# Optimization experiments

Measured on AMD Instinct MI355X. Metric: run time of the kernel, lower is better.

## Reference

```python
import jax, jax.numpy as jnp
import numpy as np

N_SRC1, N_DST1, N_DST2 = 200000, 50000, 10000
E1, E2 = 2000000, 400000
IN_F, H_F, N_CLS = 128, 256, 47


def setup_inputs() -> dict:
    key = jax.random.key(0)
    ks = jax.random.split(key, 10)
    x = jax.random.normal(ks[0], (N_SRC1, IN_F), dtype=jnp.float32)
    W_self1 = jax.random.normal(ks[1], (IN_F, H_F), dtype=jnp.float32) * (1.0 / np.sqrt(IN_F))
    W_neigh1 = jax.random.normal(ks[2], (IN_F, H_F), dtype=jnp.float32) * (1.0 / np.sqrt(IN_F))
    b1 = jnp.zeros((H_F,), dtype=jnp.float32)
    W_self2 = jax.random.normal(ks[3], (H_F, N_CLS), dtype=jnp.float32) * (1.0 / np.sqrt(H_F))
    W_neigh2 = jax.random.normal(ks[4], (H_F, N_CLS), dtype=jnp.float32) * (1.0 / np.sqrt(H_F))
    b2 = jnp.zeros((N_CLS,), dtype=jnp.float32)
    src1 = jax.random.randint(ks[5], (E1,), 0, N_SRC1, dtype=jnp.int64)
    dst1 = jnp.sort(jax.random.randint(ks[6], (E1,), 0, N_DST1, dtype=jnp.int64))
    src2 = jax.random.randint(ks[7], (E2,), 0, N_DST1, dtype=jnp.int64)
    dst2 = jnp.sort(jax.random.randint(ks[8], (E2,), 0, N_DST2, dtype=jnp.int64))
    return {"x": x, "W_self1": W_self1, "W_neigh1": W_neigh1, "b1": b1,
            "W_self2": W_self2, "W_neigh2": W_neigh2, "b2": b2,
            "src1": src1, "dst1": dst1, "src2": src2, "dst2": dst2,
            "n_dst1": N_DST1, "n_dst2": N_DST2}


def _sage_mean(h_src, h_dst, src, dst, n_dst, W_self, W_neigh, b):
    # mean neighbor aggregation: gather src feats, segment-sum onto dst, divide by in-degree
    msum = jax.ops.segment_sum(h_src[src], dst, num_segments=n_dst)  # [n_dst, F]
    deg = jax.ops.segment_sum(jnp.ones(src.shape, h_src.dtype), dst, num_segments=n_dst)
    h_neigh = msum / jnp.maximum(deg, 1.0)[:, None]
    return h_dst @ W_self + h_neigh @ W_neigh + b


def reference(x, W_self1, W_neigh1, b1, W_self2, W_neigh2, b2,
              src1, dst1, src2, dst2, n_dst1, n_dst2):
    # layer 1 (dst nodes are the prefix of src nodes, DGL MFG convention)
    h = _sage_mean(x, x[:n_dst1], src1, dst1, n_dst1, W_self1, W_neigh1, b1)
    h = jax.nn.relu(h)  # dropout = identity (eval mode)
    # layer 2
    out = _sage_mean(h, h[:n_dst2], src2, dst2, n_dst2, W_self2, W_neigh2, b2)
    return out
```

## Files before the change

kernel.cpp:

```cpp
#include <hip/hip_runtime.h>

constexpr int N_DST1 = 50000;
constexpr int N_DST2 = 10000;
constexpr int E1     = 2000000;
constexpr int E2     = 400000;
constexpr int IN_F   = 128;
constexpr int H_F    = 256;
constexpr int N_CLS  = 47;

constexpr size_t RP1_OFF = 0;
constexpr size_t RP2_OFF = 204800;
constexpr size_t BPS_OFF = 245760;
constexpr size_t BPN_OFF = 311296;
constexpr size_t BP2_OFF = 376832;
constexpr size_t X8_OFF  = 430080;
constexpr size_t HN1_OFF = 26030080;
constexpr size_t HB_OFF  = 38830080;
constexpr size_t H8_OFF  = 64430080;
constexpr size_t HN2_OFF = 77230080;

using f32x4  = __attribute__((ext_vector_type(4))) float;
using f32x2  = __attribute__((ext_vector_type(2))) float;
using short8 = __attribute__((ext_vector_type(8))) short;

__device__ __forceinline__ ushort f2bf(float f) {
    union { float f; unsigned u; } v; v.f = f;
    unsigned u = v.u;
    return (ushort)((u + 0x7fffu + ((u >> 16) & 1u)) >> 16);
}
__device__ __forceinline__ float bflo(unsigned p) {
    union { unsigned u; float f; } v; v.u = p << 16; return v.f;
}
__device__ __forceinline__ float bfhi(unsigned p) {
    union { unsigned u; float f; } v; v.u = p & 0xffff0000u; return v.f;
}

__global__ __launch_bounds__(256) void cast_x8(const float* __restrict__ x,
                                               unsigned char* __restrict__ x8) {
    int i = blockIdx.x * 256 + threadIdx.x;
    float4 v0 = ((const float4*)x)[2 * i];
    float4 v1 = ((const float4*)x)[2 * i + 1];
    int p0 = __builtin_amdgcn_cvt_pk_fp8_f32(v0.x, v0.y, 0, false);
    p0     = __builtin_amdgcn_cvt_pk_fp8_f32(v0.z, v0.w, p0, true);
    int p1 = __builtin_amdgcn_cvt_pk_fp8_f32(v1.x, v1.y, 0, false);
    p1     = __builtin_amdgcn_cvt_pk_fp8_f32(v1.z, v1.w, p1, true);
    uint2 o; o.x = (unsigned)p0; o.y = (unsigned)p1;
    ((uint2*)x8)[i] = o;
}

__global__ __launch_bounds__(256) void pack_all(
    const float* __restrict__ Ws1, const float* __restrict__ Wn1,
    const float* __restrict__ Ws2, const float* __restrict__ Wn2,
    ushort* __restrict__ bps, ushort* __restrict__ bpn,
    ushort* __restrict__ bp2) {
    int b = blockIdx.x;
    if (b < 32) {
        const float* W = (b < 16) ? Ws1 : Wn1;
        ushort* P      = (b < 16) ? bps : bpn;
        int idx = (b & 15) * 256 + threadIdx.x;
        int lane = idx & 63, kb = (idx >> 6) & 3, nb = idx >> 8;
        int n  = nb * 16 + (lane & 15);
        int k0 = kb * 32 + ((lane >> 4) * 8);
        ushort tmp[8];
#pragma unroll
        for (int j = 0; j < 8; ++j) tmp[j] = f2bf(W[(k0 + j) * H_F + n]);
        ((uint4*)P)[idx] = *(uint4*)tmp;
    } else {
        int idx = (b - 32) * 256 + threadIdx.x;
        int lane = idx & 63, rem = idx >> 6;
        int nb = rem % 3, kb = rem / 3;
        int col = nb * 16 + (lane & 15);
        int k0  = (kb & 7) * 32 + ((lane >> 4) * 8);
        const float* W = (kb < 8) ? Ws2 : Wn2;
        ushort tmp[8];
#pragma unroll
        for (int j = 0; j < 8; ++j)
            tmp[j] = (col < N_CLS) ? f2bf(W[(k0 + j) * N_CLS + col]) : (ushort)0;
        ((uint4*)bp2)[(kb * 3 + nb) * 64 + lane] = *(uint4*)tmp;
    }
}

__global__ void rowptr_all(const int* __restrict__ dst1,
                           const int* __restrict__ dst2,
                           int* __restrict__ rp1, int* __restrict__ rp2) {
    int idx = blockIdx.x * blockDim.x + threadIdx.x;
    const int* dst; int* rp; int E; int target;
    if (idx <= N_DST1) { dst = dst1; rp = rp1; E = E1; target = idx; }
    else if (idx <= N_DST1 + 1 + N_DST2) {
        dst = dst2; rp = rp2; E = E2; target = idx - (N_DST1 + 1);
    } else return;
    int lo = 0, hi = E;
    while (lo < hi) {
        int mid = (lo + hi) >> 1;
        if (dst[mid] < target) lo = mid + 1; else hi = mid;
    }
    rp[target] = lo;
}

__global__ __launch_bounds__(64) void agg1b(const unsigned char* __restrict__ x8,
                                            const int* __restrict__ src,
                                            const int* __restrict__ rp,
                                            ushort* __restrict__ hn) {
    int d = blockIdx.x, t = threadIdx.x;
    int s = rp[d], e = rp[d + 1];
    const ushort* xr = (const ushort*)x8;
    float a0 = 0.f, a1 = 0.f;
    for (int base = s; base < e; base += 64) {
        int rem = e - base;
        int n = rem < 64 ? rem : 64;
        int idx = src[base + (t < rem ? t : 0)];
        int j = 0;
        for (; j + 8 <= n; j += 8) {
            ushort u[8];
#pragma unroll
            for (int q = 0; q < 8; ++q) {
                int sq = __shfl(idx, j + q);
                u[q] = xr[sq * 64 + t];
            }
#pragma unroll
            for (int q = 0; q < 8; ++q) {
                f32x2 f = __builtin_amdgcn_cvt_pk_f32_fp8((int)u[q], false);
                a0 += f[0]; a1 += f[1];
            }
        }
        for (; j < n; ++j) {
            int sq = __shfl(idx, j);
            f32x2 f = __builtin_amdgcn_cvt_pk_f32_fp8((int)xr[sq * 64 + t], false);
            a0 += f[0]; a1 += f[1];
        }
    }
    float inv = 1.f / fmaxf((float)(e - s), 1.f);
    ((unsigned*)hn)[d * 64 + t] =
        (unsigned)f2bf(a0 * inv) | ((unsigned)f2bf(a1 * inv) << 16);
}

__global__ __launch_bounds__(64) void agg2b(const unsigned char* __restrict__ h8,
                                            const int* __restrict__ src,
                                            const int* __restrict__ rp,
                                            ushort* __restrict__ hn) {
    int d = blockIdx.x, t = threadIdx.x;
    int s = rp[d], e = rp[d + 1];
    const unsigned* hr = (const unsigned*)h8;
    float a0 = 0.f, a1 = 0.f, a2 = 0.f, a3 = 0.f;
    for (int base = s; base < e; base += 64) {
        int rem = e - base;
        int n = rem < 64 ? rem : 64;
        int idx = src[base + (t < rem ? t : 0)];
        int j = 0;
        for (; j + 4 <= n; j += 4) {
            unsigned u[4];
#pragma unroll
            for (int q = 0; q < 4; ++q) {
                int sq = __shfl(idx, j + q);
                u[q] = hr[sq * 64 + t];
            }
#pragma unroll
            for (int q = 0; q < 4; ++q) {
                f32x2 f0 = __builtin_amdgcn_cvt_pk_f32_fp8((int)u[q], false);
                f32x2 f1 = __builtin_amdgcn_cvt_pk_f32_fp8((int)u[q], true);
                a0 += f0[0]; a1 += f0[1]; a2 += f1[0]; a3 += f1[1];
            }
        }
        for (; j < n; ++j) {
            int sq = __shfl(idx, j);
            unsigned u = hr[sq * 64 + t];
            f32x2 f0 = __builtin_amdgcn_cvt_pk_f32_fp8((int)u, false);
            f32x2 f1 = __builtin_amdgcn_cvt_pk_f32_fp8((int)u, true);
            a0 += f0[0]; a1 += f0[1]; a2 += f1[0]; a3 += f1[1];
        }
    }
    float inv = 1.f / fmaxf((float)(e - s), 1.f);
    uint2 o;
    o.x = (unsigned)f2bf(a0 * inv) | ((unsigned)f2bf(a1 * inv) << 16);
    o.y = (unsigned)f2bf(a2 * inv) | ((unsigned)f2bf(a3 * inv) << 16);
    ((uint2*)hn)[d * 64 + t] = o;
}

__global__ __launch_bounds__(256) void gemm1_mfma(
    const float* __restrict__ x, const ushort* __restrict__ hn1,
    const ushort* __restrict__ BpS, const ushort* __restrict__ BpN,
    const float* __restrict__ b1, ushort* __restrict__ hb,
    unsigned char* __restrict__ h8) {
    __shared__ ushort bsm[16 * 64 * 8];
    int tid = threadIdx.x;
    int wave = tid >> 6, lane = tid & 63;
    int m0 = (blockIdx.x * 4 + wave) * 16;
    int mrow = m0 + (lane & 15);
    bool active = (m0 < N_DST1);
    if (mrow >= N_DST1) mrow = 0;
    int koff = (lane >> 4) * 8;

    f32x4 acc[16];
#pragma unroll
    for (int nb = 0; nb < 16; ++nb) acc[nb] = (f32x4){0.f, 0.f, 0.f, 0.f};

    for (int ph = 0; ph < 2; ++ph) {
        const uint4* Pg = (const uint4*)((ph == 0) ? BpS : BpN);
        const float*  Af = x   + (size_t)mrow * IN_F;
        const ushort* Ah = hn1 + (size_t)mrow * IN_F;
        for (int kb = 0; kb < 4; ++kb) {
            __syncthreads();
#pragma unroll
            for (int i = 0; i < 4; ++i) {
                int u = tid + 256 * i;
                int nb = u >> 6, l6 = u & 63;
                ((uint4*)bsm)[u] = Pg[(nb * 4 + kb) * 64 + l6];
            }
            __syncthreads();
            short8 a;
            if (ph == 0) {
                float4 a0 = *(const float4*)(Af + kb * 32 + koff);
                float4 a1 = *(const float4*)(Af + kb * 32 + koff + 4);
                a[0] = (short)f2bf(a0.x); a[1] = (short)f2bf(a0.y);
                a[2] = (short)f2bf(a0.z); a[3] = (short)f2bf(a0.w);
                a[4] = (short)f2bf(a1.x); a[5] = (short)f2bf(a1.y);
                a[6] = (short)f2bf(a1.z); a[7] = (short)f2bf(a1.w);
            } else {
                a = *(const short8*)(Ah + kb * 32 + koff);
            }
#pragma unroll
            for (int nb = 0; nb < 16; ++nb) {
                short8 b = *(const short8*)&bsm[(nb * 64 + lane) * 8];
                acc[nb] = __builtin_amdgcn_mfma_f32_16x16x32_bf16(a, b, acc[nb], 0, 0, 0);
            }
        }
    }
    if (!active) return;
    int crow0 = m0 + (lane >> 4) * 4;
    int ccol  = lane & 15;
#pragma unroll
    for (int nb = 0; nb < 16; ++nb) {
        float bias = b1[nb * 16 + ccol];
#pragma unroll
        for (int r = 0; r < 4; ++r) {
            int row = crow0 + r;
            if (row < N_DST1) {
                float v = fmaxf(acc[nb][r] + bias, 0.f);
                size_t col = (size_t)nb * 16 + ccol;
                hb[(size_t)row * H_F + col] = f2bf(v);
                int p = __builtin_amdgcn_cvt_pk_fp8_f32(v, v, 0, false);
                h8[(size_t)row * H_F + col] = (unsigned char)(p & 0xff);
            }
        }
    }
}

__global__ __launch_bounds__(256) void gemm2_mfma(
    const ushort* __restrict__ hb, const ushort* __restrict__ hn2,
    const ushort* __restrict__ P2, const float* __restrict__ b2,
    float* __restrict__ out) {
    int tid = threadIdx.x;
    int wave = tid >> 6, lane = tid & 63;
    int m0 = (blockIdx.x * 4 + wave) * 16;
    if (m0 >= N_DST2) return;
    int mrow = m0 + (lane & 15);
    int koff = (lane >> 4) * 8;

    f32x4 acc[3];
#pragma unroll
    for (int nb = 0; nb < 3; ++nb) acc[nb] = (f32x4){0.f, 0.f, 0.f, 0.f};

#pragma unroll
    for (int kb = 0; kb < 16; ++kb) {
        const ushort* A = (kb < 8)
            ? (hb  + (size_t)mrow * H_F + kb * 32 + koff)
            : (hn2 + (size_t)mrow * H_F + (kb - 8) * 32 + koff);
        short8 a = *(const short8*)A;
#pragma unroll
        for (int nb = 0; nb < 3; ++nb) {
            short8 b = *(const short8*)(P2 + ((size_t)(kb * 3 + nb) * 64 + lane) * 8);
            acc[nb] = __builtin_amdgcn_mfma_f32_16x16x32_bf16(a, b, acc[nb], 0, 0, 0);
        }
    }
    int crow0 = m0 + (lane >> 4) * 4;
    int ccol  = lane & 15;
#pragma unroll
    for (int nb = 0; nb < 3; ++nb) {
        int col = nb * 16 + ccol;
        if (col < N_CLS) {
            float bias = b2[col];
#pragma unroll
            for (int r = 0; r < 4; ++r)
                out[(size_t)(crow0 + r) * N_CLS + col] = acc[nb][r] + bias;
        }
    }
}

extern "C" void kernel_launch(void* const* d_in, const int* in_sizes, int n_in,
                              void* d_out, int out_size, void* d_ws, size_t ws_size,
                              hipStream_t stream) {
    const float* x   = (const float*)d_in[0];
    const float* Ws1 = (const float*)d_in[1];
    const float* Wn1 = (const float*)d_in[2];
    const float* b1  = (const float*)d_in[3];
    const float* Ws2 = (const float*)d_in[4];
    const float* Wn2 = (const float*)d_in[5];
    const float* b2  = (const float*)d_in[6];
    const int* src1  = (const int*)d_in[7];
    const int* dst1  = (const int*)d_in[8];
    const int* src2  = (const int*)d_in[9];
    const int* dst2  = (const int*)d_in[10];
    float* out = (float*)d_out;

    char* ws = (char*)d_ws;
    int*           rp1 = (int*)(ws + RP1_OFF);
    int*           rp2 = (int*)(ws + RP2_OFF);
    ushort*        bps = (ushort*)(ws + BPS_OFF);
    ushort*        bpn = (ushort*)(ws + BPN_OFF);
    ushort*        bp2 = (ushort*)(ws + BP2_OFF);
    unsigned char* x8  = (unsigned char*)(ws + X8_OFF);
    ushort*        hn1 = (ushort*)(ws + HN1_OFF);
    ushort*        hb  = (ushort*)(ws + HB_OFF);
    unsigned char* h8  = (unsigned char*)(ws + H8_OFF);
    ushort*        hn2 = (ushort*)(ws + HN2_OFF);

    cast_x8<<<200000 * IN_F / 8 / 256, 256, 0, stream>>>(x, x8);
    pack_all<<<44, 256, 0, stream>>>(Ws1, Wn1, Ws2, Wn2, bps, bpn, bp2);
    rowptr_all<<<(N_DST1 + N_DST2 + 2 + 255) / 256, 256, 0, stream>>>(dst1, dst2, rp1, rp2);
    agg1b<<<N_DST1, 64, 0, stream>>>(x8, src1, rp1, hn1);
    gemm1_mfma<<<(N_DST1 / 16 + 3) / 4, 256, 0, stream>>>(x, hn1, bps, bpn, b1, hb, h8);
    agg2b<<<N_DST2, 64, 0, stream>>>(h8, src2, rp2, hn2);
    gemm2_mfma<<<(N_DST2 / 16 + 3) / 4, 256, 0, stream>>>(hb, hn2, bp2, b2, out);
}
```

Measured before the change: 311.6 us.

## Merge setup kernels and gather two neighbors per wave with wider loads

The cast, weight-pack and row-pointer kernels are merged into one launch, which removes two kernel launches and their gaps. Both aggregation kernels now split the 64-lane wave into two halves. Each half gathers a different neighbor's row using wider per-lane loads (4 or 8 bytes) and reads src indices directly instead of through shuffles, and the two halves are combined with a cross-half shuffle at the end. This is meant to issue fewer, wider memory requests and keep more gathers in flight per wave. The cost is a final reduction step, and half of the wave sits idle when a node has an odd degree.

Result: no change. 306.6 us (-1.6%).

```diff
diff --git a/kernel.cpp b/kernel.cpp
--- a/kernel.cpp
+++ b/kernel.cpp
@@ -28,73 +28,71 @@
     unsigned u = v.u;
     return (ushort)((u + 0x7fffu + ((u >> 16) & 1u)) >> 16);
 }
-__device__ __forceinline__ float bflo(unsigned p) {
-    union { unsigned u; float f; } v; v.u = p << 16; return v.f;
-}
-__device__ __forceinline__ float bfhi(unsigned p) {
-    union { unsigned u; float f; } v; v.u = p & 0xffff0000u; return v.f;
-}
-
-__global__ __launch_bounds__(256) void cast_x8(const float* __restrict__ x,
-                                               unsigned char* __restrict__ x8) {
-    int i = blockIdx.x * 256 + threadIdx.x;
-    float4 v0 = ((const float4*)x)[2 * i];
-    float4 v1 = ((const float4*)x)[2 * i + 1];
-    int p0 = __builtin_amdgcn_cvt_pk_fp8_f32(v0.x, v0.y, 0, false);
-    p0     = __builtin_amdgcn_cvt_pk_fp8_f32(v0.z, v0.w, p0, true);
-    int p1 = __builtin_amdgcn_cvt_pk_fp8_f32(v1.x, v1.y, 0, false);
-    p1     = __builtin_amdgcn_cvt_pk_fp8_f32(v1.z, v1.w, p1, true);
-    uint2 o; o.x = (unsigned)p0; o.y = (unsigned)p1;
-    ((uint2*)x8)[i] = o;
-}
-
-__global__ __launch_bounds__(256) void pack_all(
+
+constexpr int CAST_BLKS = 200000 * IN_F / 8 / 256;
+constexpr int PACK_BLKS = 44;
+constexpr int RP_BLKS   = (N_DST1 + N_DST2 + 2 + 255) / 256;
+
+__global__ __launch_bounds__(256) void setup_all(
+    const float* __restrict__ x, unsigned char* __restrict__ x8,
     const float* __restrict__ Ws1, const float* __restrict__ Wn1,
     const float* __restrict__ Ws2, const float* __restrict__ Wn2,
-    ushort* __restrict__ bps, ushort* __restrict__ bpn,
-    ushort* __restrict__ bp2) {
+    ushort* __restrict__ bps, ushort* __restrict__ bpn, ushort* __restrict__ bp2,
+    const int* __restrict__ dst1, const int* __restrict__ dst2,
+    int* __restrict__ rp1, int* __restrict__ rp2) {
     int b = blockIdx.x;
-    if (b < 32) {
-        const float* W = (b < 16) ? Ws1 : Wn1;
-        ushort* P      = (b < 16) ? bps : bpn;
-        int idx = (b & 15) * 256 + threadIdx.x;
-        int lane = idx & 63, kb = (idx >> 6) & 3, nb = idx >> 8;
-        int n  = nb * 16 + (lane & 15);
-        int k0 = kb * 32 + ((lane >> 4) * 8);
-        ushort tmp[8];
-#pragma unroll
-        for (int j = 0; j < 8; ++j) tmp[j] = f2bf(W[(k0 + j) * H_F + n]);
-        ((uint4*)P)[idx] = *(uint4*)tmp;
+    if (b < CAST_BLKS) {
+        int i = b * 256 + threadIdx.x;
+        float4 v0 = ((const float4*)x)[2 * i];
+        float4 v1 = ((const float4*)x)[2 * i + 1];
+        int p0 = __builtin_amdgcn_cvt_pk_fp8_f32(v0.x, v0.y, 0, false);
+        p0     = __builtin_amdgcn_cvt_pk_fp8_f32(v0.z, v0.w, p0, true);
+        int p1 = __builtin_amdgcn_cvt_pk_fp8_f32(v1.x, v1.y, 0, false);
+        p1     = __builtin_amdgcn_cvt_pk_fp8_f32(v1.z, v1.w, p1, true);
+        uint2 o; o.x = (unsigned)p0; o.y = (unsigned)p1;
+        ((uint2*)x8)[i] = o;
+    } else if (b < CAST_BLKS + PACK_BLKS) {
+        int pb = b - CAST_BLKS;
+        if (pb < 32) {
+            const float* W = (pb < 16) ? Ws1 : Wn1;
+            ushort* P      = (pb < 16) ? bps : bpn;
+            int idx = (pb & 15) * 256 + threadIdx.x;
+            int lane = idx & 63, kb = (idx >> 6) & 3, nb = idx >> 8;
+            int n  = nb * 16 + (lane & 15);
+            int k0 = kb * 32 + ((lane >> 4) * 8);
+            ushort tmp[8];
+#pragma unroll
+            for (int j = 0; j < 8; ++j) tmp[j] = f2bf(W[(k0 + j) * H_F + n]);
+            ((uint4*)P)[idx] = *(uint4*)tmp;
+        } else {
+            int idx = (pb - 32) * 256 + threadIdx.x;
+            if (idx < 3072) {
+                int lane = idx & 63, rem = idx >> 6;
+                int nb = rem % 3, kb = rem / 3;
+                int col = nb * 16 + (lane & 15);
+                int k0  = (kb & 7) * 32 + ((lane >> 4) * 8);
+                const float* W = (kb < 8) ? Ws2 : Wn2;
+                ushort tmp[8];
+#pragma unroll
+                for (int j = 0; j < 8; ++j)
+                    tmp[j] = (col < N_CLS) ? f2bf(W[(k0 + j) * N_CLS + col]) : (ushort)0;
+                ((uint4*)bp2)[(kb * 3 + nb) * 64 + lane] = *(uint4*)tmp;
+            }
+        }
     } else {
-        int idx = (b - 32) * 256 + threadIdx.x;
-        int lane = idx & 63, rem = idx >> 6;
-        int nb = rem % 3, kb = rem / 3;
-        int col = nb * 16 + (lane & 15);
-        int k0  = (kb & 7) * 32 + ((lane >> 4) * 8);
-        const float* W = (kb < 8) ? Ws2 : Wn2;
-        ushort tmp[8];
-#pragma unroll
-        for (int j = 0; j < 8; ++j)
-            tmp[j] = (col < N_CLS) ? f2bf(W[(k0 + j) * N_CLS + col]) : (ushort)0;
-        ((uint4*)bp2)[(kb * 3 + nb) * 64 + lane] = *(uint4*)tmp;
-    }
-}
-
-__global__ void rowptr_all(const int* __restrict__ dst1,
-                           const int* __restrict__ dst2,
-                           int* __restrict__ rp1, int* __restrict__ rp2) {
-    int idx = blockIdx.x * blockDim.x + threadIdx.x;
-    const int* dst; int* rp; int E; int target;
-    if (idx <= N_DST1) { dst = dst1; rp = rp1; E = E1; target = idx; }
-    else if (idx <= N_DST1 + 1 + N_DST2) {
-        dst = dst2; rp = rp2; E = E2; target = idx - (N_DST1 + 1);
-    } else return;
-    int lo = 0, hi = E;
-    while (lo < hi) {
-        int mid = (lo + hi) >> 1;
-        if (dst[mid] < target) lo = mid + 1; else hi = mid;
-    }
-    rp[target] = lo;
+        int idx = (b - CAST_BLKS - PACK_BLKS) * 256 + threadIdx.x;
+        const int* dst; int* rp; int E; int target;
+        if (idx <= N_DST1) { dst = dst1; rp = rp1; E = E1; target = idx; }
+        else if (idx <= N_DST1 + 1 + N_DST2) {
+            dst = dst2; rp = rp2; E = E2; target = idx - (N_DST1 + 1);
+        } else return;
+        int lo = 0, hi = E;
+        while (lo < hi) {
+            int mid = (lo + hi) >> 1;
+            if (dst[mid] < target) lo = mid + 1; else hi = mid;
+        }
+        rp[target] = lo;
+    }
 }
 
 __global__ __launch_bounds__(64) void agg1b(const unsigned char* __restrict__ x8,
@@ -103,35 +101,56 @@
                                             ushort* __restrict__ hn) {
     int d = blockIdx.x, t = threadIdx.x;
     int s = rp[d], e = rp[d + 1];
-    const ushort* xr = (const ushort*)x8;
-    float a0 = 0.f, a1 = 0.f;
-    for (int base = s; base < e; base += 64) {
-        int rem = e - base;
-        int n = rem < 64 ? rem : 64;
-        int idx = src[base + (t < rem ? t : 0)];
-        int j = 0;
-        for (; j + 8 <= n; j += 8) {
-            ushort u[8];
-#pragma unroll
-            for (int q = 0; q < 8; ++q) {
-                int sq = __shfl(idx, j + q);
-                u[q] = xr[sq * 64 + t];
-            }
-#pragma unroll
-            for (int q = 0; q < 8; ++q) {
-                f32x2 f = __builtin_amdgcn_cvt_pk_f32_fp8((int)u[q], false);
-                a0 += f[0]; a1 += f[1];
-            }
-        }
-        for (; j < n; ++j) {
-            int sq = __shfl(idx, j);
-            f32x2 f = __builtin_amdgcn_cvt_pk_f32_fp8((int)xr[sq * 64 + t], false);
-            a0 += f[0]; a1 += f[1];
-        }
-    }
-    float inv = 1.f / fmaxf((float)(e - s), 1.f);
-    ((unsigned*)hn)[d * 64 + t] =
-        (unsigned)f2bf(a0 * inv) | ((unsigned)f2bf(a1 * inv) << 16);
+    const unsigned* x1 = (const unsigned*)x8;
+    int half = t >> 5, li = t & 31;
+    float a0 = 0.f, a1 = 0.f, a2 = 0.f, a3 = 0.f;
+    int deg = e - s;
+    int npairs = deg >> 1;
+    int j = 0;
+    for (; j + 4 <= npairs; j += 4) {
+        int b0 = s + 2 * j;
+        int i0 = src[b0],     i1 = src[b0 + 1], i2 = src[b0 + 2], i3 = src[b0 + 3];
+        int i4 = src[b0 + 4], i5 = src[b0 + 5], i6 = src[b0 + 6], i7 = src[b0 + 7];
+        unsigned v0 = x1[(half ? i1 : i0) * 32 + li];
+        unsigned v1 = x1[(half ? i3 : i2) * 32 + li];
+        unsigned v2 = x1[(half ? i5 : i4) * 32 + li];
+        unsigned v3 = x1[(half ? i7 : i6) * 32 + li];
+#pragma unroll
+        for (int q = 0; q < 4; ++q) {
+            unsigned v = (q == 0) ? v0 : (q == 1) ? v1 : (q == 2) ? v2 : v3;
+            f32x2 f0 = __builtin_amdgcn_cvt_pk_f32_fp8((int)v, false);
+            f32x2 f1 = __builtin_amdgcn_cvt_pk_f32_fp8((int)v, true);
+            a0 += f0[0]; a1 += f0[1]; a2 += f1[0]; a3 += f1[1];
+        }
+    }
+    for (; j < npairs; ++j) {
+        int b0 = s + 2 * j;
+        int i0 = src[b0], i1 = src[b0 + 1];
+        unsigned v = x1[(half ? i1 : i0) * 32 + li];
+        f32x2 f0 = __builtin_amdgcn_cvt_pk_f32_fp8((int)v, false);
+        f32x2 f1 = __builtin_amdgcn_cvt_pk_f32_fp8((int)v, true);
+        a0 += f0[0]; a1 += f0[1]; a2 += f1[0]; a3 += f1[1];
+    }
+    if (deg & 1) {
+        int it = src[e - 1];
+        if (half == 0) {
+            unsigned v = x1[it * 32 + li];
+            f32x2 f0 = __builtin_amdgcn_cvt_pk_f32_fp8((int)v, false);
+            f32x2 f1 = __builtin_amdgcn_cvt_pk_f32_fp8((int)v, true);
+            a0 += f0[0]; a1 += f0[1]; a2 += f1[0]; a3 += f1[1];
+        }
+    }
+    float c0 = a0 + __shfl(a0, li + 32);
+    float c1 = a1 + __shfl(a1, li + 32);
+    float c2 = a2 + __shfl(a2, li + 32);
+    float c3 = a3 + __shfl(a3, li + 32);
+    if (t < 32) {
+        float inv = 1.f / fmaxf((float)deg, 1.f);
+        uint2 o;
+        o.x = (unsigned)f2bf(c0 * inv) | ((unsigned)f2bf(c1 * inv) << 16);
+        o.y = (unsigned)f2bf(c2 * inv) | ((unsigned)f2bf(c3 * inv) << 16);
+        ((uint2*)hn)[d * 32 + li] = o;
+    }
 }
 
 __global__ __launch_bounds__(64) void agg2b(const unsigned char* __restrict__ h8,
@@ -140,40 +159,63 @@
                                             ushort* __restrict__ hn) {
     int d = blockIdx.x, t = threadIdx.x;
     int s = rp[d], e = rp[d + 1];
-    const unsigned* hr = (const unsigned*)h8;
-    float a0 = 0.f, a1 = 0.f, a2 = 0.f, a3 = 0.f;
-    for (int base = s; base < e; base += 64) {
-        int rem = e - base;
-        int n = rem < 64 ? rem : 64;
-        int idx = src[base + (t < rem ? t : 0)];
-        int j = 0;
-        for (; j + 4 <= n; j += 4) {
-            unsigned u[4];
-#pragma unroll
-            for (int q = 0; q < 4; ++q) {
-                int sq = __shfl(idx, j + q);
-                u[q] = hr[sq * 64 + t];
-            }
-#pragma unroll
-            for (int q = 0; q < 4; ++q) {
-                f32x2 f0 = __builtin_amdgcn_cvt_pk_f32_fp8((int)u[q], false);
-                f32x2 f1 = __builtin_amdgcn_cvt_pk_f32_fp8((int)u[q], true);
-                a0 += f0[0]; a1 += f0[1]; a2 += f1[0]; a3 += f1[1];
-            }
-        }
-        for (; j < n; ++j) {
-            int sq = __shfl(idx, j);
-            unsigned u = hr[sq * 64 + t];
-            f32x2 f0 = __builtin_amdgcn_cvt_pk_f32_fp8((int)u, false);
-            f32x2 f1 = __builtin_amdgcn_cvt_pk_f32_fp8((int)u, true);
-            a0 += f0[0]; a1 += f0[1]; a2 += f1[0]; a3 += f1[1];
-        }
-    }
-    float inv = 1.f / fmaxf((float)(e - s), 1.f);
-    uint2 o;
-    o.x = (unsigned)f2bf(a0 * inv) | ((unsigned)f2bf(a1 * inv) << 16);
-    o.y = (unsigned)f2bf(a2 * inv) | ((unsigned)f2bf(a3 * inv) << 16);
-    ((uint2*)hn)[d * 64 + t] = o;
+    const uint2* h2 = (const uint2*)h8;
+    int half = t >> 5, li = t & 31;
+    float a[8] = {};
+    int deg = e - s;
+    int npairs = deg >> 1;
+    int j = 0;
+    for (; j + 2 <= npairs; j += 2) {
+        int b0 = s + 2 * j;
+        int i0 = src[b0], i1 = src[b0 + 1], i2 = src[b0 + 2], i3 = src[b0 + 3];
+        uint2 v0 = h2[(half ? i1 : i0) * 32 + li];
+        uint2 v1 = h2[(half ? i3 : i2) * 32 + li];
+#pragma unroll
+        for (int q = 0; q < 2; ++q) {
+            uint2 v = q ? v1 : v0;
+            f32x2 f0 = __builtin_amdgcn_cvt_pk_f32_fp8((int)v.x, false);
+            f32x2 f1 = __builtin_amdgcn_cvt_pk_f32_fp8((int)v.x, true);
+            f32x2 f2 = __builtin_amdgcn_cvt_pk_f32_fp8((int)v.y, false);
+            f32x2 f3 = __builtin_amdgcn_cvt_pk_f32_fp8((int)v.y, true);
+            a[0] += f0[0]; a[1] += f0[1]; a[2] += f1[0]; a[3] += f1[1];
+            a[4] += f2[0]; a[5] += f2[1]; a[6] += f3[0]; a[7] += f3[1];
+        }
+    }
+    for (; j < npairs; ++j) {
+        int b0 = s + 2 * j;
+        int i0 = src[b0], i1 = src[b0 + 1];
+        uint2 v = h2[(half ? i1 : i0) * 32 + li];
+        f32x2 f0 = __builtin_amdgcn_cvt_pk_f32_fp8((int)v.x, false);
+        f32x2 f1 = __builtin_amdgcn_cvt_pk_f32_fp8((int)v.x, true);
+        f32x2 f2 = __builtin_amdgcn_cvt_pk_f32_fp8((int)v.y, false);
+        f32x2 f3 = __builtin_amdgcn_cvt_pk_f32_fp8((int)v.y, true);
+        a[0] += f0[0]; a[1] += f0[1]; a[2] += f1[0]; a[3] += f1[1];
+        a[4] += f2[0]; a[5] += f2[1]; a[6] += f3[0]; a[7] += f3[1];
+    }
+    if (deg & 1) {
+        int it = src[e - 1];
+        if (half == 0) {
+            uint2 v = h2[it * 32 + li];
+            f32x2 f0 = __builtin_amdgcn_cvt_pk_f32_fp8((int)v.x, false);
+            f32x2 f1 = __builtin_amdgcn_cvt_pk_f32_fp8((int)v.x, true);
+            f32x2 f2 = __builtin_amdgcn_cvt_pk_f32_fp8((int)v.y, false);
+            f32x2 f3 = __builtin_amdgcn_cvt_pk_f32_fp8((int)v.y, true);
+            a[0] += f0[0]; a[1] += f0[1]; a[2] += f1[0]; a[3] += f1[1];
+            a[4] += f2[0]; a[5] += f2[1]; a[6] += f3[0]; a[7] += f3[1];
+        }
+    }
+    float c[8];
+#pragma unroll
+    for (int q = 0; q < 8; ++q) c[q] = a[q] + __shfl(a[q], li + 32);
+    if (t < 32) {
+        float inv = 1.f / fmaxf((float)deg, 1.f);
+        uint4 o;
+        o.x = (unsigned)f2bf(c[0] * inv) | ((unsigned)f2bf(c[1] * inv) << 16);
+        o.y = (unsigned)f2bf(c[2] * inv) | ((unsigned)f2bf(c[3] * inv) << 16);
+        o.z = (unsigned)f2bf(c[4] * inv) | ((unsigned)f2bf(c[5] * inv) << 16);
+        o.w = (unsigned)f2bf(c[6] * inv) | ((unsigned)f2bf(c[7] * inv) << 16);
+        ((uint4*)hn)[d * 32 + li] = o;
+    }
 }
 
 __global__ __launch_bounds__(256) void gemm1_mfma(
@@ -314,9 +356,8 @@
     unsigned char* h8  = (unsigned char*)(ws + H8_OFF);
     ushort*        hn2 = (ushort*)(ws + HN2_OFF);
 
-    cast_x8<<<200000 * IN_F / 8 / 256, 256, 0, stream>>>(x, x8);
-    pack_all<<<44, 256, 0, stream>>>(Ws1, Wn1, Ws2, Wn2, bps, bpn, bp2);
-    rowptr_all<<<(N_DST1 + N_DST2 + 2 + 255) / 256, 256, 0, stream>>>(dst1, dst2, rp1, rp2);
+    setup_all<<<CAST_BLKS + PACK_BLKS + RP_BLKS, 256, 0, stream>>>(
+        x, x8, Ws1, Wn1, Ws2, Wn2, bps, bpn, bp2, dst1, dst2, rp1, rp2);
     agg1b<<<N_DST1, 64, 0, stream>>>(x8, src1, rp1, hn1);
     gemm1_mfma<<<(N_DST1 / 16 + 3) / 4, 256, 0, stream>>>(x, hn1, bps, bpn, b1, hb, h8);
     agg2b<<<N_DST2, 64, 0, stream>>>(h8, src2, rp2, hn2);
```
